# Performance work log

Measured on AMD Instinct MI355X. Metric: run time of the kernel, lower is better.

The kernel has to match this reference:

```python
import jax, jax.numpy as jnp
import numpy as np
from itertools import permutations

B, S, D = 1024, 16, 128
G_DIMS = [256, 256]
F_DIMS = [256, 256]

# all ordered pairs (i, j), i != j, in the same lexicographic order as
# itertools.permutations used by the torch module
_PAIRS = np.array(list(permutations(range(S), 2)), dtype=np.int32)  # [P, 2], P = S*(S-1)


def _init_linear(key, in_dim, out_dim):
    kw, kb = jax.random.split(key)
    bound = 1.0 / np.sqrt(in_dim)
    W = jax.random.uniform(kw, (in_dim, out_dim), jnp.float32, -bound, bound)
    b = jax.random.uniform(kb, (out_dim,), jnp.float32, -bound, bound)
    return W, b


def setup_inputs() -> dict:
    key = jax.random.key(0)
    ks = jax.random.split(key, 5)
    state = jax.random.normal(ks[0], (B, S, D), jnp.float32)
    gW0, gb0 = _init_linear(ks[1], 2 * D, G_DIMS[0])
    gW1, gb1 = _init_linear(ks[2], G_DIMS[0], G_DIMS[1])
    fW0, fb0 = _init_linear(ks[3], G_DIMS[1], F_DIMS[0])
    fW1, fb1 = _init_linear(ks[4], F_DIMS[0], F_DIMS[1])
    return {"state": state,
            "gW0": gW0, "gb0": gb0, "gW1": gW1, "gb1": gb1,
            "fW0": fW0, "fb0": fb0, "fW1": fW1, "fb1": fb1}


def reference(state, gW0, gb0, gW1, gb1, fW0, fb0, fW1, fb1):
    i_idx = jnp.asarray(_PAIRS[:, 0])
    j_idx = jnp.asarray(_PAIRS[:, 1])
    # gather + concat all ordered pairs: [B, P, 2D]
    paired = jnp.concatenate([state[:, i_idx], state[:, j_idx]], axis=-1)
    # g-MLP applied per pair
    h = jax.nn.relu(jnp.einsum('bpd,de->bpe', paired, gW0) + gb0)
    h = jax.nn.relu(jnp.einsum('bpd,de->bpe', h, gW1) + gb1)
    # sum over pairs -> [B, g_out]
    pooled = h.sum(axis=1)
    # f-MLP
    out = jax.nn.relu(pooled @ fW0 + fb0)
    out = jax.nn.relu(out @ fW1 + fb1)
    return out
```

## Files before the change

### kernel.cpp

```cpp
#include <hip/hip_runtime.h>

typedef __attribute__((ext_vector_type(8))) _Float16 f16x8;
typedef __attribute__((ext_vector_type(4))) float f32x4;

#define HSTR 264

__global__ __launch_bounds__(256) void prep_kernel(
    const float* __restrict__ gW0, const float* __restrict__ gW1,
    _Float16* __restrict__ W0c, _Float16* __restrict__ W1c)
{
  const int t = blockIdx.x * 256 + threadIdx.x;
  {
    const int c = t >> 7, k = t & 127;
    const int dst = ((k >> 5) * 32 + (c >> 4)) * 512 +
                    (((k >> 3) & 3) * 16 + (c & 15)) * 8 + (k & 7);
    const int src = (k + ((c >= 256) ? 128 : 0)) * 256 + (c & 255);
    W0c[dst] = (_Float16)gW0[src];
  }
  {
    const int n = t >> 8, k = t & 255;
    const int dst = ((k >> 5) * 16 + (n >> 4)) * 512 +
                    (((k >> 3) & 3) * 16 + (n & 15)) * 8 + (k & 7);
    W1c[dst] = (_Float16)gW1[k * 256 + n];
  }
}

__global__ __launch_bounds__(512, 4) void pair_kernel(
    const float* __restrict__ state,
    const _Float16* __restrict__ W0c, const float* __restrict__ gb0,
    const _Float16* __restrict__ W1c, const float* __restrict__ gb1,
    float* __restrict__ pooled)
{
  const int b   = blockIdx.x;
  const int tid = threadIdx.x;
  const int w   = tid >> 6;
  const int l   = tid & 63;
  const int lr  = l & 15;
  const int lg  = l >> 4;

  __shared__ __align__(16) char smem[8448 + 32768];
  _Float16* A_lds = (_Float16*)smem;
  char*     ubuf  = smem + 8448;
  _Float16* C_st  = (_Float16*)ubuf;

  const float* stb = state + (size_t)b * 2048;

  f16x8 sfrag[4];
  #pragma unroll
  for (int kk = 0; kk < 4; ++kk) {
    const float* sp = stb + lr * 128 + kk * 32 + lg * 8;
    f32x4 s0 = *(const f32x4*)sp;
    f32x4 s1 = *(const f32x4*)(sp + 4);
    f16x8 f;
    f[0] = (_Float16)s0[0]; f[1] = (_Float16)s0[1];
    f[2] = (_Float16)s0[2]; f[3] = (_Float16)s0[3];
    f[4] = (_Float16)s1[0]; f[5] = (_Float16)s1[1];
    f[6] = (_Float16)s1[2]; f[7] = (_Float16)s1[3];
    sfrag[kk] = f;
  }

  const f32x4 z4 = {0.f, 0.f, 0.f, 0.f};
  f32x4 acc2[4];
  #pragma unroll
  for (int nt = 0; nt < 4; ++nt) acc2[nt] = z4;

  #pragma unroll
  for (int nt = 0; nt < 4; ++nt) {
    #pragma unroll
    for (int kk = 0; kk < 4; ++kk) {
      f16x8 bf = *(const f16x8*)(W0c + (size_t)((kk * 32 + 4 * w + nt) * 512 + l * 8));
      acc2[nt] = __builtin_amdgcn_mfma_f32_16x16x32_f16(sfrag[kk], bf, acc2[nt], 0, 0, 0);
    }
  }

  f16x8 bw[2][8];
  #pragma unroll
  for (int nt = 0; nt < 2; ++nt) {
    #pragma unroll
    for (int kk = 0; kk < 8; ++kk) {
      bw[nt][kk] = *(const f16x8*)(W1c + (size_t)((kk * 16 + 2 * w + nt) * 512 + l * 8));
      asm volatile("" : "+a"(bw[nt][kk]));
    }
  }
  float gb1v[2];
  gb1v[0] = gb1[32 * w + lr];
  gb1v[1] = gb1[32 * w + 16 + lr];

  #pragma unroll
  for (int nt = 0; nt < 4; ++nt) {
    const int col = 64 * w + 16 * nt + lr;
    #pragma unroll
    for (int r = 0; r < 4; ++r) {
      const int row = lg * 4 + r;
      const float v = acc2[nt][r];
      if (col < 256) A_lds[row * HSTR + col]       = (_Float16)(v + gb0[col]);
      else           C_st[row * HSTR + col - 256]  = (_Float16)v;
    }
  }
  __syncthreads();

  const int kh = (w & 1) * 4;
  f16x8 creg[4];
  #pragma unroll
  for (int kq = 0; kq < 4; ++kq)
    creg[kq] = *(const f16x8*)&C_st[lr * HSTR + (kh + kq) * 32 + lg * 8];
  __syncthreads();

  const f16x8 zh = {(_Float16)0, (_Float16)0, (_Float16)0, (_Float16)0,
                    (_Float16)0, (_Float16)0, (_Float16)0, (_Float16)0};

  const int tc = w >> 1;
  float pp0 = 0.f, pp1 = 0.f;

  #pragma unroll 1
  for (int g = 0; g < 4; ++g) {
    {
      const int ip = 4 * g + tc;
      char* tb = ubuf + tc * 8192;
      #pragma unroll
      for (int kq = 0; kq < 4; ++kq) {
        const int kk = kh + kq;
        f16x8 av = *(const f16x8*)&A_lds[ip * HSTR + kk * 32 + lg * 8];
        f16x8 u = __builtin_elementwise_max(av + creg[kq], zh);
        *(f16x8*)(tb + kk * 1024 + l * 16) = u;
      }
    }
    __syncthreads();

    #pragma unroll
    for (int t = 0; t < 4; ++t) {
      const char* tb = ubuf + t * 8192;
      f32x4 a0 = z4, a1 = z4;
      #pragma unroll
      for (int kk = 0; kk < 8; ++kk) {
        f16x8 uf = *(const f16x8*)(tb + kk * 1024 + l * 16);
        a0 = __builtin_amdgcn_mfma_f32_16x16x32_f16(uf, bw[0][kk], a0, 0, 0, 0);
        a1 = __builtin_amdgcn_mfma_f32_16x16x32_f16(uf, bw[1][kk], a1, 0, 0, 0);
      }
      const int i = 4 * g + t;
      #pragma unroll
      for (int r = 0; r < 4; ++r) {
        const int row = lg * 4 + r;
        const float v0 = fmaxf(a0[r] + gb1v[0], 0.f);
        const float v1 = fmaxf(a1[r] + gb1v[1], 0.f);
        pp0 += (row == i) ? 0.f : v0;
        pp1 += (row == i) ? 0.f : v1;
      }
    }
    __syncthreads();
  }

  {
    float v = pp0;
    v += __shfl_xor(v, 16);
    v += __shfl_xor(v, 32);
    if (lg == 0) pooled[(size_t)b * 256 + 32 * w + lr] = v;
  }
  {
    float v = pp1;
    v += __shfl_xor(v, 16);
    v += __shfl_xor(v, 32);
    if (lg == 0) pooled[(size_t)b * 256 + 32 * w + 16 + lr] = v;
  }
}

__global__ __launch_bounds__(256) void fmlp_kernel(
    const float* __restrict__ pooled,
    const float* __restrict__ fW0, const float* __restrict__ fb0,
    const float* __restrict__ fW1, const float* __restrict__ fb1,
    float* __restrict__ out)
{
  const int tid = threadIdx.x;
  const size_t b0 = (size_t)blockIdx.x * 4;
  __shared__ float pl[4][256];
  __shared__ float h1[4][256];

  #pragma unroll
  for (int q = 0; q < 4; ++q)
    pl[q][tid] = pooled[(b0 + q) * 256 + tid];
  __syncthreads();

  float acc[4] = {0.f, 0.f, 0.f, 0.f};
  #pragma unroll 8
  for (int k = 0; k < 256; ++k) {
    const float wv = fW0[(size_t)k * 256 + tid];
    #pragma unroll
    for (int q = 0; q < 4; ++q) acc[q] = fmaf(pl[q][k], wv, acc[q]);
  }
  #pragma unroll
  for (int q = 0; q < 4; ++q) h1[q][tid] = fmaxf(acc[q] + fb0[tid], 0.f);
  __syncthreads();

  float acc2[4] = {0.f, 0.f, 0.f, 0.f};
  #pragma unroll 8
  for (int k = 0; k < 256; ++k) {
    const float wv = fW1[(size_t)k * 256 + tid];
    #pragma unroll
    for (int q = 0; q < 4; ++q) acc2[q] = fmaf(h1[q][k], wv, acc2[q]);
  }
  #pragma unroll
  for (int q = 0; q < 4; ++q)
    out[(b0 + q) * 256 + tid] = fmaxf(acc2[q] + fb1[tid], 0.f);
}

extern "C" void kernel_launch(void* const* d_in, const int* in_sizes, int n_in,
                              void* d_out, int out_size, void* d_ws, size_t ws_size,
                              hipStream_t stream) {
  const float* state = (const float*)d_in[0];
  const float* gW0   = (const float*)d_in[1];
  const float* gb0   = (const float*)d_in[2];
  const float* gW1   = (const float*)d_in[3];
  const float* gb1   = (const float*)d_in[4];
  const float* fW0   = (const float*)d_in[5];
  const float* fb0   = (const float*)d_in[6];
  const float* fW1   = (const float*)d_in[7];
  const float* fb1   = (const float*)d_in[8];
  float* out = (float*)d_out;

  _Float16* W0c = (_Float16*)d_ws;
  _Float16* W1c = W0c + 65536;
  float* pooled = (float*)(W1c + 65536);

  const int Bn = in_sizes[0] / 2048;

  prep_kernel<<<dim3(256), dim3(256), 0, stream>>>(gW0, gW1, W0c, W1c);
  pair_kernel<<<dim3(Bn), dim3(512), 0, stream>>>(state, W0c, gb0, W1c, gb1, pooled);
  fmlp_kernel<<<dim3(Bn / 4), dim3(256), 0, stream>>>(pooled, fW0, fb0, fW1, fb1, out);
}
```

Before: 70.78 us.

## Double-buffer pair tiles in LDS and interleave two tiles' MFMA chains

Splits the LDS staging area into two buffers so the ReLU'd pair tile for the next i-group is built while the current group's MFMAs run. This removes one block-wide barrier per iteration. The inner loop also processes two tiles at once with four independent accumulators to raise MFMA-level parallelism. The cost is doubling the LDS footprint per block, which can reduce the number of resident blocks per CU.

```diff
diff --git a/kernel.cpp b/kernel.cpp
--- a/kernel.cpp
+++ b/kernel.cpp
@@ -38,10 +38,11 @@
   const int lr  = l & 15;
   const int lg  = l >> 4;
 
-  __shared__ __align__(16) char smem[8448 + 32768];
+  __shared__ __align__(16) char smem[8448 + 65536];
   _Float16* A_lds = (_Float16*)smem;
-  char*     ubuf  = smem + 8448;
-  _Float16* C_st  = (_Float16*)ubuf;
+  char*     buf0  = smem + 8448;
+  char*     buf1  = buf0 + 32768;
+  _Float16* C_st  = (_Float16*)buf1;
 
   const float* stb = state + (size_t)b * 2048;
 
@@ -104,19 +105,32 @@
   #pragma unroll
   for (int kq = 0; kq < 4; ++kq)
     creg[kq] = *(const f16x8*)&C_st[lr * HSTR + (kh + kq) * 32 + lg * 8];
-  __syncthreads();
 
   const f16x8 zh = {(_Float16)0, (_Float16)0, (_Float16)0, (_Float16)0,
                     (_Float16)0, (_Float16)0, (_Float16)0, (_Float16)0};
-
   const int tc = w >> 1;
+
+  {
+    char* tb = buf0 + tc * 8192;
+    #pragma unroll
+    for (int kq = 0; kq < 4; ++kq) {
+      const int kk = kh + kq;
+      f16x8 av = *(const f16x8*)&A_lds[tc * HSTR + kk * 32 + lg * 8];
+      f16x8 u = __builtin_elementwise_max(av + creg[kq], zh);
+      *(f16x8*)(tb + kk * 1024 + l * 16) = u;
+    }
+  }
+  __syncthreads();
+
   float pp0 = 0.f, pp1 = 0.f;
 
   #pragma unroll 1
   for (int g = 0; g < 4; ++g) {
-    {
-      const int ip = 4 * g + tc;
-      char* tb = ubuf + tc * 8192;
+    char* cbuf = (g & 1) ? buf1 : buf0;
+    if (g < 3) {
+      char* nb = (g & 1) ? buf0 : buf1;
+      const int ip = 4 * (g + 1) + tc;
+      char* tb = nb + tc * 8192;
       #pragma unroll
       for (int kq = 0; kq < 4; ++kq) {
         const int kk = kh + kq;
@@ -125,26 +139,34 @@
         *(f16x8*)(tb + kk * 1024 + l * 16) = u;
       }
     }
-    __syncthreads();
-
-    #pragma unroll
-    for (int t = 0; t < 4; ++t) {
-      const char* tb = ubuf + t * 8192;
-      f32x4 a0 = z4, a1 = z4;
+
+    #pragma unroll
+    for (int tp = 0; tp < 2; ++tp) {
+      const char* tb0 = cbuf + (2 * tp)     * 8192;
+      const char* tb1 = cbuf + (2 * tp + 1) * 8192;
+      f32x4 a00 = z4, a01 = z4, a10 = z4, a11 = z4;
       #pragma unroll
       for (int kk = 0; kk < 8; ++kk) {
-        f16x8 uf = *(const f16x8*)(tb + kk * 1024 + l * 16);
-        a0 = __builtin_amdgcn_mfma_f32_16x16x32_f16(uf, bw[0][kk], a0, 0, 0, 0);
-        a1 = __builtin_amdgcn_mfma_f32_16x16x32_f16(uf, bw[1][kk], a1, 0, 0, 0);
+        f16x8 u0 = *(const f16x8*)(tb0 + kk * 1024 + l * 16);
+        f16x8 u1 = *(const f16x8*)(tb1 + kk * 1024 + l * 16);
+        a00 = __builtin_amdgcn_mfma_f32_16x16x32_f16(u0, bw[0][kk], a00, 0, 0, 0);
+        a10 = __builtin_amdgcn_mfma_f32_16x16x32_f16(u1, bw[0][kk], a10, 0, 0, 0);
+        a01 = __builtin_amdgcn_mfma_f32_16x16x32_f16(u0, bw[1][kk], a01, 0, 0, 0);
+        a11 = __builtin_amdgcn_mfma_f32_16x16x32_f16(u1, bw[1][kk], a11, 0, 0, 0);
       }
-      const int i = 4 * g + t;
+      const int i0 = 4 * g + 2 * tp;
+      const int i1 = i0 + 1;
       #pragma unroll
       for (int r = 0; r < 4; ++r) {
         const int row = lg * 4 + r;
-        const float v0 = fmaxf(a0[r] + gb1v[0], 0.f);
-        const float v1 = fmaxf(a1[r] + gb1v[1], 0.f);
-        pp0 += (row == i) ? 0.f : v0;
-        pp1 += (row == i) ? 0.f : v1;
+        const float v00 = fmaxf(a00[r] + gb1v[0], 0.f);
+        const float v01 = fmaxf(a01[r] + gb1v[1], 0.f);
+        const float v10 = fmaxf(a10[r] + gb1v[0], 0.f);
+        const float v11 = fmaxf(a11[r] + gb1v[1], 0.f);
+        pp0 += (row == i0) ? 0.f : v00;
+        pp1 += (row == i0) ? 0.f : v01;
+        pp0 += (row == i1) ? 0.f : v10;
+        pp1 += (row == i1) ? 0.f : v11;
       }
     }
     __syncthreads();
```

Result: slower. 99.04 us (+39.9%).

## Fuse f-MLP into pair kernel, eliminating pooled buffer and third launch

Applied to the files above, without the earlier changes.

Moves the two-layer f-MLP into the tail of the pair kernel so each block computes its row's output directly from the pooled vector kept in shared memory. This removes the pooled global write/read and one kernel launch. In exchange every block now streams the full fp32 fW0/fW1 weights for a single row (no reuse across batch rows), which increases cache traffic and lengthens the tail of each block.

```diff
diff --git a/kernel.cpp b/kernel.cpp
--- a/kernel.cpp
+++ b/kernel.cpp
@@ -29,7 +29,9 @@
     const float* __restrict__ state,
     const _Float16* __restrict__ W0c, const float* __restrict__ gb0,
     const _Float16* __restrict__ W1c, const float* __restrict__ gb1,
-    float* __restrict__ pooled)
+    const float* __restrict__ fW0, const float* __restrict__ fb0,
+    const float* __restrict__ fW1, const float* __restrict__ fb1,
+    float* __restrict__ out)
 {
   const int b   = blockIdx.x;
   const int tid = threadIdx.x;
@@ -150,57 +152,58 @@
     __syncthreads();
   }
 
+  float* pool = (float*)ubuf;
+  float* part = pool + 256;
+  float* h1v  = part + 512;
   {
     float v = pp0;
     v += __shfl_xor(v, 16);
     v += __shfl_xor(v, 32);
-    if (lg == 0) pooled[(size_t)b * 256 + 32 * w + lr] = v;
+    if (lg == 0) pool[32 * w + lr] = v;
   }
   {
     float v = pp1;
     v += __shfl_xor(v, 16);
     v += __shfl_xor(v, 32);
-    if (lg == 0) pooled[(size_t)b * 256 + 32 * w + 16 + lr] = v;
-  }
-}
-
-__global__ __launch_bounds__(256) void fmlp_kernel(
-    const float* __restrict__ pooled,
-    const float* __restrict__ fW0, const float* __restrict__ fb0,
-    const float* __restrict__ fW1, const float* __restrict__ fb1,
-    float* __restrict__ out)
-{
-  const int tid = threadIdx.x;
-  const size_t b0 = (size_t)blockIdx.x * 4;
-  __shared__ float pl[4][256];
-  __shared__ float h1[4][256];
-
-  #pragma unroll
-  for (int q = 0; q < 4; ++q)
-    pl[q][tid] = pooled[(b0 + q) * 256 + tid];
-  __syncthreads();
-
-  float acc[4] = {0.f, 0.f, 0.f, 0.f};
-  #pragma unroll 8
-  for (int k = 0; k < 256; ++k) {
-    const float wv = fW0[(size_t)k * 256 + tid];
-    #pragma unroll
-    for (int q = 0; q < 4; ++q) acc[q] = fmaf(pl[q][k], wv, acc[q]);
-  }
-  #pragma unroll
-  for (int q = 0; q < 4; ++q) h1[q][tid] = fmaxf(acc[q] + fb0[tid], 0.f);
-  __syncthreads();
-
-  float acc2[4] = {0.f, 0.f, 0.f, 0.f};
-  #pragma unroll 8
-  for (int k = 0; k < 256; ++k) {
-    const float wv = fW1[(size_t)k * 256 + tid];
-    #pragma unroll
-    for (int q = 0; q < 4; ++q) acc2[q] = fmaf(h1[q][k], wv, acc2[q]);
-  }
-  #pragma unroll
-  for (int q = 0; q < 4; ++q)
-    out[(b0 + q) * 256 + tid] = fmaxf(acc2[q] + fb1[tid], 0.f);
+    if (lg == 0) pool[32 * w + 16 + lr] = v;
+  }
+  __syncthreads();
+
+  const int col = tid & 255;
+  const int kb  = tid >> 8;
+  {
+    const float* wp = fW0 + (size_t)(kb * 128) * 256 + col;
+    const float* pv = pool + kb * 128;
+    float a0 = 0.f, a1 = 0.f, a2 = 0.f, a3 = 0.f;
+    #pragma unroll 4
+    for (int k = 0; k < 128; k += 4) {
+      a0 = fmaf(pv[k + 0], wp[(size_t)(k + 0) * 256], a0);
+      a1 = fmaf(pv[k + 1], wp[(size_t)(k + 1) * 256], a1);
+      a2 = fmaf(pv[k + 2], wp[(size_t)(k + 2) * 256], a2);
+      a3 = fmaf(pv[k + 3], wp[(size_t)(k + 3) * 256], a3);
+    }
+    part[kb * 256 + col] = (a0 + a1) + (a2 + a3);
+  }
+  __syncthreads();
+  if (tid < 256) h1v[tid] = fmaxf(part[tid] + part[256 + tid] + fb0[tid], 0.f);
+  __syncthreads();
+  {
+    const float* wp = fW1 + (size_t)(kb * 128) * 256 + col;
+    const float* hv = h1v + kb * 128;
+    float a0 = 0.f, a1 = 0.f, a2 = 0.f, a3 = 0.f;
+    #pragma unroll 4
+    for (int k = 0; k < 128; k += 4) {
+      a0 = fmaf(hv[k + 0], wp[(size_t)(k + 0) * 256], a0);
+      a1 = fmaf(hv[k + 1], wp[(size_t)(k + 1) * 256], a1);
+      a2 = fmaf(hv[k + 2], wp[(size_t)(k + 2) * 256], a2);
+      a3 = fmaf(hv[k + 3], wp[(size_t)(k + 3) * 256], a3);
+    }
+    part[kb * 256 + col] = (a0 + a1) + (a2 + a3);
+  }
+  __syncthreads();
+  if (tid < 256)
+    out[(size_t)b * 256 + tid] =
+        fmaxf(part[tid] + part[256 + tid] + fb1[tid], 0.f);
 }
 
 extern "C" void kernel_launch(void* const* d_in, const int* in_sizes, int n_in,
@@ -219,11 +222,10 @@
 
   _Float16* W0c = (_Float16*)d_ws;
   _Float16* W1c = W0c + 65536;
-  float* pooled = (float*)(W1c + 65536);
 
   const int Bn = in_sizes[0] / 2048;
 
   prep_kernel<<<dim3(256), dim3(256), 0, stream>>>(gW0, gW1, W0c, W1c);
-  pair_kernel<<<dim3(Bn), dim3(512), 0, stream>>>(state, W0c, gb0, W1c, gb1, pooled);
-  fmlp_kernel<<<dim3(Bn / 4), dim3(256), 0, stream>>>(pooled, fW0, fb0, fW1, fb1, out);
+  pair_kernel<<<dim3(Bn), dim3(512), 0, stream>>>(
+      state, W0c, gb0, W1c, gb1, fW0, fb0, fW1, fb1, out);
 }
```

Result: slower. 72.85 us (+2.9%).
